# Optimization experiments

Measured on AMD Instinct MI355X. Metric: run time of the kernel, lower is better.

## Reference

```python
import jax, jax.numpy as jnp
import numpy as np

MARGIN = 0.2  # init margin
B, D = 4096, 512


def _pairwise_dist(x):
    # torch.cdist(x, x, p=2): Euclidean distance via Gram matrix
    sq = jnp.sum(x * x, axis=-1)                      # [B]
    gram = x @ x.T                                    # [B, B]
    d2 = jnp.maximum(sq[:, None] + sq[None, :] - 2.0 * gram, 0.0)
    safe = jnp.where(d2 > 0, d2, 1.0)                 # grad-safe sqrt at 0
    return jnp.where(d2 > 0, jnp.sqrt(safe), 0.0)


def setup_inputs() -> dict:
    key = jax.random.key(0)
    k1, k2, k3 = jax.random.split(key, 3)
    anchor = jax.random.normal(k1, (B, D), dtype=jnp.float32)
    positive = jax.random.normal(k2, (B, D), dtype=jnp.float32)
    labels = jax.random.randint(k3, (B,), 0, 64)
    return {"anchor": anchor, "positive": positive, "labels": labels}


def reference(anchor, positive, labels):
    d_ap = jnp.sum((anchor - positive) ** 2, axis=-1)          # [B] squared dist
    pd = _pairwise_dist(anchor)                                 # [B, B] euclidean
    diff_label = labels[None, :] != labels[:, None]             # [B, B]
    inf = jnp.float32(jnp.inf)
    # negatives farther than the positive (note: pd is euclidean, d_ap squared,
    # exactly as in the original code)
    cand = jnp.where(diff_label & (pd > d_ap[:, None]), pd, inf)
    min_larger = jnp.min(cand, axis=1)
    # fallback: min over all different-label negatives
    fallback = jnp.min(jnp.where(diff_label, pd, inf), axis=1)
    d_an = jnp.where(jnp.isfinite(min_larger), min_larger, fallback)
    loss = jnp.maximum(d_ap - d_an + MARGIN, 0.0)
    return jnp.mean(loss)
```

## Files before the change

kernel.cpp:

```cpp
#include <hip/hip_runtime.h>
#include <hip/hip_bf16.h>
#include <cstdint>
#include <cstddef>

constexpr int BN = 4096;
constexpr int DN = 512;
constexpr int NT = BN / 128;
constexpr int NBLK = NT * (NT + 1) / 2;
constexpr float MARGIN = 0.2f;
constexpr uint32_t INF_U = 0x7f800000u;

typedef __attribute__((ext_vector_type(8))) short short8;
typedef __attribute__((ext_vector_type(4))) float float4v;

__global__ __launch_bounds__(256) void prep_kernel(
    const float* __restrict__ anchor,
    const float* __restrict__ positive,
    const int* __restrict__ labels,
    uint16_t* __restrict__ Abf,
    float4* __restrict__ meta,
    uint32_t* __restrict__ min_all,
    uint32_t* __restrict__ min_larger,
    uint32_t* __restrict__ done_count)
{
    const int tid  = threadIdx.x;
    const int wave = tid >> 6;
    const int lane = tid & 63;
    const int row  = blockIdx.x * 4 + wave;

    if (blockIdx.x == 0 && tid == 0) *done_count = 0;

    const float4* arow = (const float4*)(anchor   + (size_t)row * DN);
    const float4* prow = (const float4*)(positive + (size_t)row * DN);

    float4 av0 = arow[lane * 2 + 0], av1 = arow[lane * 2 + 1];
    float4 pv0 = prow[lane * 2 + 0], pv1 = prow[lane * 2 + 1];

    float a[8] = {av0.x, av0.y, av0.z, av0.w, av1.x, av1.y, av1.z, av1.w};
    float p[8] = {pv0.x, pv0.y, pv0.z, pv0.w, pv1.x, pv1.y, pv1.z, pv1.w};

    float s = 0.f, d = 0.f;
    union { uint16_t u[8]; uint4 v; } pk;
    #pragma unroll
    for (int i = 0; i < 8; ++i) {
        s += a[i] * a[i];
        float dx = a[i] - p[i];
        d += dx * dx;
        uint32_t ub = __float_as_uint(a[i]);
        pk.u[i] = (uint16_t)((ub + 0x7fffu + ((ub >> 16) & 1u)) >> 16);
    }

    ((uint4*)(Abf + (size_t)row * DN))[lane] = pk.v;

    #pragma unroll
    for (int off = 32; off; off >>= 1) {
        s += __shfl_xor(s, off);
        d += __shfl_xor(d, off);
    }
    if (lane == 0) {
        meta[row] = (float4){s, d, d * d, __uint_as_float((uint32_t)labels[row])};
        min_all[row]    = INF_U;
        min_larger[row] = INF_U;
    }
}

__global__ __launch_bounds__(256, 3) void gram_kernel(
    const uint16_t* __restrict__ Abf,
    const float4* __restrict__ meta,
    uint32_t* __restrict__ min_all,
    uint32_t* __restrict__ min_larger,
    uint32_t* __restrict__ done_count,
    float* __restrict__ out)
{
    __shared__ uint16_t Abuf[128 * 64];
    __shared__ uint16_t Bbuf[128 * 64];

    int t = blockIdx.x, bi = 0, rem = NT;
    while (t >= rem) { t -= rem; ++bi; --rem; }
    const int bj = bi + t;
    const bool offdiag = (bi != bj);
    const int rowBase = bi * 128;
    const int colBase = bj * 128;

    const int tid  = threadIdx.x;
    const int wave = tid >> 6;
    const int lane = tid & 63;
    const int wi   = wave >> 1;
    const int wj   = wave & 1;
    const int quad = lane >> 4;
    const int l15  = lane & 15;

    int sr[4], sc[4], sp[4];
    #pragma unroll
    for (int i = 0; i < 4; ++i) {
        int l = tid + i * 256;
        sr[i] = l >> 3; sc[i] = l & 7; sp[i] = sc[i] ^ (sr[i] & 7);
    }

    float4v acc[4][4];
    #pragma unroll
    for (int i = 0; i < 4; ++i)
        #pragma unroll
        for (int j = 0; j < 4; ++j)
            acc[i][j] = (float4v){0.f, 0.f, 0.f, 0.f};

    for (int kt = 0; kt < DN / 64; ++kt) {
        const int k0 = kt * 64;
        __syncthreads();
        {
            uint4 st[4];
            #pragma unroll
            for (int i = 0; i < 4; ++i)
                st[i] = *(const uint4*)(Abf + (size_t)(rowBase + sr[i]) * DN + k0 + sc[i] * 8);
            #pragma unroll
            for (int i = 0; i < 4; ++i)
                *(uint4*)(Abuf + sr[i] * 64 + sp[i] * 8) = st[i];
            #pragma unroll
            for (int i = 0; i < 4; ++i)
                st[i] = *(const uint4*)(Abf + (size_t)(colBase + sr[i]) * DN + k0 + sc[i] * 8);
            #pragma unroll
            for (int i = 0; i < 4; ++i)
                *(uint4*)(Bbuf + sr[i] * 64 + sp[i] * 8) = st[i];
        }
        __syncthreads();

        #pragma unroll
        for (int kk = 0; kk < 2; ++kk) {
            short8 af[4], bfr[4];
            #pragma unroll
            for (int mi = 0; mi < 4; ++mi) {
                int r = wi * 64 + mi * 16 + l15;
                int p = (kk * 4 + quad) ^ (r & 7);
                af[mi] = *(const short8*)(Abuf + r * 64 + p * 8);
            }
            #pragma unroll
            for (int mj = 0; mj < 4; ++mj) {
                int r = wj * 64 + mj * 16 + l15;
                int p = (kk * 4 + quad) ^ (r & 7);
                bfr[mj] = *(const short8*)(Bbuf + r * 64 + p * 8);
            }
            #pragma unroll
            for (int mi = 0; mi < 4; ++mi)
                #pragma unroll
                for (int mj = 0; mj < 4; ++mj)
                    acc[mi][mj] = __builtin_amdgcn_mfma_f32_16x16x32_bf16(
                        af[mi], bfr[mj], acc[mi][mj], 0, 0, 0);
        }
    }

    const float INFF = __uint_as_float(INF_U);
    float4 mj_meta[4];
    #pragma unroll
    for (int mj = 0; mj < 4; ++mj)
        mj_meta[mj] = meta[colBase + wj * 64 + mj * 16 + l15];

    float cAll[4], cLarger[4];
    #pragma unroll
    for (int mj = 0; mj < 4; ++mj) { cAll[mj] = INFF; cLarger[mj] = INFF; }

    #pragma unroll
    for (int mi = 0; mi < 4; ++mi) {
        #pragma unroll
        for (int r = 0; r < 4; ++r) {
            int row = rowBase + wi * 64 + mi * 16 + quad * 4 + r;
            float4 mim = meta[row];
            uint32_t li = __float_as_uint(mim.w);
            float mAll = INFF, mLarger = INFF;
            #pragma unroll
            for (int mj = 0; mj < 4; ++mj) {
                float d2 = mim.x + mj_meta[mj].x - 2.0f * acc[mi][mj][r];
                d2 = d2 > 0.f ? d2 : 0.f;
                if (__float_as_uint(mj_meta[mj].w) != li) {
                    mAll = fminf(mAll, d2);
                    if (d2 > mim.z) mLarger = fminf(mLarger, d2);
                    if (offdiag) {
                        cAll[mj] = fminf(cAll[mj], d2);
                        if (d2 > mj_meta[mj].z) cLarger[mj] = fminf(cLarger[mj], d2);
                    }
                }
            }
            #pragma unroll
            for (int off = 1; off < 16; off <<= 1) {
                mAll    = fminf(mAll,    __shfl_xor(mAll, off));
                mLarger = fminf(mLarger, __shfl_xor(mLarger, off));
            }
            if (l15 == 0) {
                atomicMin(&min_all[row],    __float_as_uint(mAll));
                atomicMin(&min_larger[row], __float_as_uint(mLarger));
            }
        }
    }
    if (offdiag) {
        #pragma unroll
        for (int mj = 0; mj < 4; ++mj) {
            float a0 = cAll[mj], l0 = cLarger[mj];
            a0 = fminf(a0, __shfl_xor(a0, 16)); l0 = fminf(l0, __shfl_xor(l0, 16));
            a0 = fminf(a0, __shfl_xor(a0, 32)); l0 = fminf(l0, __shfl_xor(l0, 32));
            if (quad == 0) {
                int col = colBase + wj * 64 + mj * 16 + l15;
                atomicMin(&min_all[col],    __float_as_uint(a0));
                atomicMin(&min_larger[col], __float_as_uint(l0));
            }
        }
    }

    __shared__ bool isLast;
    __syncthreads();
    if (tid == 0) {
        __threadfence();
        isLast = (atomicAdd(done_count, 1u) == NBLK - 1);
    }
    __syncthreads();
    if (isLast) {
        __threadfence();
        float s = 0.f;
        for (int i = tid; i < BN; i += 256) {
            uint32_t mlu = __hip_atomic_load(&min_larger[i], __ATOMIC_RELAXED, __HIP_MEMORY_SCOPE_AGENT);
            uint32_t mau = __hip_atomic_load(&min_all[i],    __ATOMIC_RELAXED, __HIP_MEMORY_SCOPE_AGENT);
            float dan2 = (mlu != INF_U) ? __uint_as_float(mlu) : __uint_as_float(mau);
            float l = meta[i].y - sqrtf(dan2) + MARGIN;
            s += l > 0.f ? l : 0.f;
        }
        #pragma unroll
        for (int off = 32; off; off >>= 1) s += __shfl_xor(s, off);
        __shared__ float wsum[4];
        if ((tid & 63) == 0) wsum[tid >> 6] = s;
        __syncthreads();
        if (tid == 0) out[0] = (wsum[0] + wsum[1] + wsum[2] + wsum[3]) * (1.0f / BN);
    }
}

extern "C" void kernel_launch(void* const* d_in, const int* in_sizes, int n_in,
                              void* d_out, int out_size, void* d_ws, size_t ws_size,
                              hipStream_t stream) {
    const float* anchor   = (const float*)d_in[0];
    const float* positive = (const float*)d_in[1];
    const int*   labels   = (const int*)d_in[2];
    float* out = (float*)d_out;

    uint8_t* ws = (uint8_t*)d_ws;
    uint16_t* Abf        = (uint16_t*)ws;
    float4*   meta       = (float4*)(ws + (size_t)BN * DN * 2);
    uint32_t* min_all    = (uint32_t*)(meta + BN);
    uint32_t* min_larger = min_all + BN;
    uint32_t* done_count = min_larger + BN;

    prep_kernel<<<BN / 4, 256, 0, stream>>>(anchor, positive, labels, Abf, meta,
                                            min_all, min_larger, done_count);
    gram_kernel<<<NBLK, 256, 0, stream>>>(Abf, meta, min_all, min_larger, done_count, out);
}
```

Before: 106.6 us.

## Load MFMA fragments directly from global memory with register double buffering

Drops the shared-memory staging of the A and B tiles, so each wave loads its bf16 MFMA fragments straight from global memory into registers. The next k-step's fragments are prefetched into a second register buffer while MFMAs run on the current one, and the block-wide barriers go away. In exchange each wave reloads data that other waves also need, which raises global/L2 traffic, and the 16-byte per-lane row-strided loads are less coalesced. Register pressure also rises, which may hurt occupancy under the 3-blocks-per-CU launch bound.

```diff
diff --git a/kernel.cpp b/kernel.cpp
--- a/kernel.cpp
+++ b/kernel.cpp
@@ -72,9 +72,6 @@
     uint32_t* __restrict__ done_count,
     float* __restrict__ out)
 {
-    __shared__ uint16_t Abuf[128 * 64];
-    __shared__ uint16_t Bbuf[128 * 64];
-
     int t = blockIdx.x, bi = 0, rem = NT;
     while (t >= rem) { t -= rem; ++bi; --rem; }
     const int bj = bi + t;
@@ -90,12 +87,8 @@
     const int quad = lane >> 4;
     const int l15  = lane & 15;
 
-    int sr[4], sc[4], sp[4];
-    #pragma unroll
-    for (int i = 0; i < 4; ++i) {
-        int l = tid + i * 256;
-        sr[i] = l >> 3; sc[i] = l & 7; sp[i] = sc[i] ^ (sr[i] & 7);
-    }
+    const uint16_t* aBase = Abf + (size_t)(rowBase + wi * 64 + l15) * DN + quad * 8;
+    const uint16_t* bBase = Abf + (size_t)(colBase + wj * 64 + l15) * DN + quad * 8;
 
     float4v acc[4][4];
     #pragma unroll
@@ -104,48 +97,29 @@
         for (int j = 0; j < 4; ++j)
             acc[i][j] = (float4v){0.f, 0.f, 0.f, 0.f};
 
-    for (int kt = 0; kt < DN / 64; ++kt) {
-        const int k0 = kt * 64;
-        __syncthreads();
-        {
-            uint4 st[4];
-            #pragma unroll
-            for (int i = 0; i < 4; ++i)
-                st[i] = *(const uint4*)(Abf + (size_t)(rowBase + sr[i]) * DN + k0 + sc[i] * 8);
-            #pragma unroll
-            for (int i = 0; i < 4; ++i)
-                *(uint4*)(Abuf + sr[i] * 64 + sp[i] * 8) = st[i];
-            #pragma unroll
-            for (int i = 0; i < 4; ++i)
-                st[i] = *(const uint4*)(Abf + (size_t)(colBase + sr[i]) * DN + k0 + sc[i] * 8);
-            #pragma unroll
-            for (int i = 0; i < 4; ++i)
-                *(uint4*)(Bbuf + sr[i] * 64 + sp[i] * 8) = st[i];
-        }
-        __syncthreads();
-
-        #pragma unroll
-        for (int kk = 0; kk < 2; ++kk) {
-            short8 af[4], bfr[4];
-            #pragma unroll
-            for (int mi = 0; mi < 4; ++mi) {
-                int r = wi * 64 + mi * 16 + l15;
-                int p = (kk * 4 + quad) ^ (r & 7);
-                af[mi] = *(const short8*)(Abuf + r * 64 + p * 8);
-            }
-            #pragma unroll
-            for (int mj = 0; mj < 4; ++mj) {
-                int r = wj * 64 + mj * 16 + l15;
-                int p = (kk * 4 + quad) ^ (r & 7);
-                bfr[mj] = *(const short8*)(Bbuf + r * 64 + p * 8);
-            }
-            #pragma unroll
-            for (int mi = 0; mi < 4; ++mi)
-                #pragma unroll
-                for (int mj = 0; mj < 4; ++mj)
-                    acc[mi][mj] = __builtin_amdgcn_mfma_f32_16x16x32_bf16(
-                        af[mi], bfr[mj], acc[mi][mj], 0, 0, 0);
-        }
+    short8 fA[2][4], fB[2][4];
+    #pragma unroll
+    for (int m = 0; m < 4; ++m) {
+        fA[0][m] = *(const short8*)(aBase + m * 16 * DN);
+        fB[0][m] = *(const short8*)(bBase + m * 16 * DN);
+    }
+
+    #pragma unroll
+    for (int kt = 0; kt < DN / 32; ++kt) {
+        const int cur = kt & 1, nxt = cur ^ 1;
+        if (kt < DN / 32 - 1) {
+            #pragma unroll
+            for (int m = 0; m < 4; ++m) {
+                fA[nxt][m] = *(const short8*)(aBase + m * 16 * DN + (kt + 1) * 32);
+                fB[nxt][m] = *(const short8*)(bBase + m * 16 * DN + (kt + 1) * 32);
+            }
+        }
+        #pragma unroll
+        for (int mi = 0; mi < 4; ++mi)
+            #pragma unroll
+            for (int mj = 0; mj < 4; ++mj)
+                acc[mi][mj] = __builtin_amdgcn_mfma_f32_16x16x32_bf16(
+                    fA[cur][mi], fB[cur][mj], acc[mi][mj], 0, 0, 0);
     }
 
     const float INFF = __uint_as_float(INF_U);
```

New measurement: 136.6 us. 28.2% more time.
